# Optimization experiments

Measured on AMD Instinct MI355X. Metric: run time of the kernel, lower is better.

## Reference

```python
import jax, jax.numpy as jnp
import numpy as np

N, E = 50000, 800000
DIM_IN, DIM_H, DIM_OUT, HEADS = 128, 32, 16, 4
HID = DIM_H * HEADS  # 128
FINAL = DIM_OUT * HEADS  # 64
NEG_SLOPE = 0.2


def _glorot(key, shape):
    fan_in, fan_out = shape[0], shape[-1] if len(shape) > 1 else shape[0]
    lim = jnp.sqrt(6.0 / (fan_in + fan_out)).astype(jnp.float32)
    return jax.random.uniform(key, shape, jnp.float32, -lim, lim)


def setup_inputs() -> dict:
    key = jax.random.key(0)
    ks = jax.random.split(key, 16)
    x = jax.random.normal(ks[0], (N, DIM_IN), jnp.float32)
    edge_index = jax.random.randint(ks[1], (2, E), 0, N, dtype=jnp.int64)
    inp = {"x": x, "edge_index": edge_index}
    # layer 1: DIM_IN -> HEADS*DIM_H
    inp["Wl1"] = _glorot(ks[2], (DIM_IN, HEADS * DIM_H))
    inp["Wr1"] = _glorot(ks[3], (DIM_IN, HEADS * DIM_H))
    inp["att1"] = _glorot(ks[4], (HEADS, DIM_H))
    inp["b1"] = jnp.zeros((HEADS * DIM_H,), jnp.float32)
    # layer 2: HID -> HEADS*DIM_H
    inp["Wl2"] = _glorot(ks[5], (HID, HEADS * DIM_H))
    inp["Wr2"] = _glorot(ks[6], (HID, HEADS * DIM_H))
    inp["att2"] = _glorot(ks[7], (HEADS, DIM_H))
    inp["b2"] = jnp.zeros((HEADS * DIM_H,), jnp.float32)
    # layer 3: HID -> HEADS*DIM_OUT
    inp["Wl3"] = _glorot(ks[8], (HID, HEADS * DIM_OUT))
    inp["Wr3"] = _glorot(ks[9], (HID, HEADS * DIM_OUT))
    inp["att3"] = _glorot(ks[10], (HEADS, DIM_OUT))
    inp["b3"] = jnp.zeros((HEADS * DIM_OUT,), jnp.float32)
    return inp


def gatv2_conv(x, src, dst, Wl, Wr, att, b, heads, ch):
    n = x.shape[0]
    xl = (x @ Wl).reshape(n, heads, ch)  # source-side transform
    xr = (x @ Wr).reshape(n, heads, ch)  # target-side transform
    m = xl[src] + xr[dst]                 # [E, H, C]
    e = jnp.einsum('ehc,hc->eh', jax.nn.leaky_relu(m, NEG_SLOPE), att)
    # segment softmax over incoming edges of each dst node
    emax = jax.ops.segment_max(e, dst, num_segments=n)
    ex = jnp.exp(e - emax[dst])
    denom = jax.ops.segment_sum(ex, dst, num_segments=n)
    alpha = ex / denom[dst]               # [E, H]
    out = jax.ops.segment_sum(alpha[:, :, None] * xl[src], dst, num_segments=n)
    return out.reshape(n, heads * ch) + b


def reference(x, edge_index, Wl1, Wr1, att1, b1, Wl2, Wr2, att2, b2, Wl3, Wr3, att3, b3):
    n = x.shape[0]
    loops = jnp.arange(n, dtype=edge_index.dtype)
    src = jnp.concatenate([edge_index[0], loops])  # PyG add_self_loops=True
    dst = jnp.concatenate([edge_index[1], loops])
    # dropout is identity in eval mode
    h = jax.nn.elu(gatv2_conv(x, src, dst, Wl1, Wr1, att1, b1, HEADS, DIM_H))
    h = jax.nn.elu(gatv2_conv(h, src, dst, Wl2, Wr2, att2, b2, HEADS, DIM_H))
    h = gatv2_conv(h, src, dst, Wl3, Wr3, att3, b3, HEADS, DIM_OUT)
    return jax.nn.log_softmax(h, axis=1)
```

## Files before the change

### kernel.cpp

```cpp
#include <hip/hip_runtime.h>
#include <math.h>

constexpr int DIN  = 128;
constexpr int FSH  = 10;
constexpr int NFBM = 64;
constexpr int LCAP = 160;
constexpr int RND  = 4096;
constexpr int FCAP = 18432;

typedef __attribute__((ext_vector_type(8))) short short8;
typedef __attribute__((ext_vector_type(4))) float f32x4;

__device__ __forceinline__ unsigned short f2bf(float f) {
  unsigned u = __float_as_uint(f);
  u = (u + 0x7FFF + ((u >> 16) & 1)) >> 16;
  return (unsigned short)u;
}
__device__ __forceinline__ float bflo(unsigned u) { return __uint_as_float(u << 16); }
__device__ __forceinline__ float bfhi(unsigned u) { return __uint_as_float(u & 0xFFFF0000u); }

__device__ __forceinline__ void unpack8(uint4 u, float* x) {
  x[0] = bflo(u.x); x[1] = bfhi(u.x); x[2] = bflo(u.y); x[3] = bfhi(u.y);
  x[4] = bflo(u.z); x[5] = bfhi(u.z); x[6] = bflo(u.w); x[7] = bfhi(u.w);
}
__device__ __forceinline__ void unpack4(uint2 u, float* x) {
  x[0] = bflo(u.x); x[1] = bfhi(u.x); x[2] = bflo(u.y); x[3] = bfhi(u.y);
}

typedef const __attribute__((address_space(1))) unsigned int guint_t;
typedef __attribute__((address_space(3))) unsigned int luint_t;
__device__ __forceinline__ void async16(const void* g, void* l) {
  __builtin_amdgcn_global_load_lds((guint_t*)g, (luint_t*)l, 16, 0, 0);
}


__global__ __launch_bounds__(256) void bucket_append_kernel(const int* __restrict__ ei,
    int* __restrict__ gcnt, unsigned* __restrict__ gpairs, int E, int nfb) {
  __shared__ unsigned buf[NFBM * LCAP];
  __shared__ int cnt[NFBM];
  __shared__ int gbase[NFBM];
  const int tid = threadIdx.x;
  if (tid < NFBM) cnt[tid] = 0;
  __syncthreads();

  const int k0 = blockIdx.x * RND;
  for (int i = tid; i < RND; i += 256) {
    int k = k0 + i;
    if (k >= E) break;
    int src = ei[k], dst = ei[E + k];
    int fb = dst >> FSH;
    int pos = atomicAdd(&cnt[fb], 1);
    if (pos < LCAP)
      buf[fb * LCAP + pos] = (unsigned)src | ((unsigned)(dst & ((1 << FSH) - 1)) << 16);
  }
  __syncthreads();

  if (tid < nfb) gbase[tid] = atomicAdd(&gcnt[tid], min(cnt[tid], LCAP));
  __syncthreads();

  const int wid = tid >> 6, lane = tid & 63;
  for (int fb = wid; fb < nfb; fb += 4) {
    int c  = min(cnt[fb], LCAP);
    int gb = gbase[fb];
    if (gb >= FCAP) continue;
    c = min(c, FCAP - gb);
    unsigned* dstp = gpairs + (size_t)fb * FCAP + gb;
    const unsigned* srcp = &buf[fb * LCAP];
    for (int i = lane; i < c; i += 64) dstp[i] = srcp[i];
  }
}

__global__ __launch_bounds__(256) void bucket_build_kernel(const unsigned* __restrict__ gpairs,
    const int* __restrict__ gcnt, int* __restrict__ row_ptr,
    int* __restrict__ edge_src, int n, int nfb) {
  const int b   = blockIdx.x;
  const int tid = threadIdx.x;
  const int lane = tid & 63, wid = tid >> 6;
  __shared__ int hist[1024];
  __shared__ int wsum[4];
  __shared__ int base_s;

  const int d0 = b << FSH;
  const int nvalid = min(1 << FSH, n - d0);

  if (wid == 0) {
    int term = 0;
    if (lane < b)
      term = min(gcnt[lane], FCAP) + min(1 << FSH, n - (lane << FSH));
#pragma unroll
    for (int o = 32; o >= 1; o >>= 1) term += __shfl_xor(term, o, 64);
    if (lane == 0) base_s = term;
  }
  for (int i = tid; i < 1024; i += 256) hist[i] = (i < nvalid) ? 1 : 0;
  __syncthreads();

  const int cnt = min(gcnt[b], FCAP);
  const unsigned* bp = gpairs + (size_t)b * FCAP;
  for (int i = tid; i < cnt; i += 256)
    atomicAdd(&hist[bp[i] >> 16], 1);
  __syncthreads();

  const int i4 = tid * 4;
  int h0 = hist[i4], h1 = hist[i4 + 1], h2 = hist[i4 + 2], h3 = hist[i4 + 3];
  int s = h0 + h1 + h2 + h3;
  int incl = s;
#pragma unroll
  for (int o = 1; o < 64; o <<= 1) {
    int t = __shfl_up(incl, o, 64);
    if (lane >= o) incl += t;
  }
  if (lane == 63) wsum[wid] = incl;
  __syncthreads();
  int wo = 0;
  for (int wq = 0; wq < wid; ++wq) wo += wsum[wq];
  const int base = base_s;
  int ex[4];
  ex[0] = wo + incl - s;
  ex[1] = ex[0] + h0;
  ex[2] = ex[1] + h1;
  ex[3] = ex[2] + h2;
#pragma unroll
  for (int j = 0; j < 4; ++j) {
    int d = i4 + j;
    if (d < nvalid) {
      row_ptr[d0 + d] = base + ex[j];
      edge_src[base + ex[j]] = d0 + d;
      hist[d] = ex[j] + 1;
    } else if (d0 + d == n) {
      row_ptr[n] = base + ex[j];
    }
  }
  if (b == nfb - 1 && d0 + 1024 <= n && tid == 0) row_ptr[n] = base + cnt + nvalid;
  __syncthreads();

  for (int i = tid; i < cnt; i += 256) {
    unsigned p = bp[i];
    int pos = atomicAdd(&hist[p >> 16], 1);
    edge_src[base + pos] = (int)(p & 0xFFFFu);
  }
}

__global__ __launch_bounds__(256) void cvt_w_kernel(
    const float* __restrict__ Wl1, const float* __restrict__ Wr1,
    const float* __restrict__ Wl2, const float* __restrict__ Wr2,
    const float* __restrict__ Wl3, const float* __restrict__ Wr3,
    unsigned short* __restrict__ Wt) {
  int e = blockIdx.x * 256 + threadIdx.x;
  if (e >= 81920) return;
  const float* src; int N; int off;
  if (e < 65536) {
    int m = e >> 14; off = e & 16383; N = 128;
    src = (m == 0) ? Wl1 : (m == 1) ? Wr1 : (m == 2) ? Wl2 : Wr2;
  } else {
    int e2 = e - 65536; int m = e2 >> 13; off = e2 & 8191; N = 64;
    src = m ? Wr3 : Wl3;
  }
  int nn = off >> 7, k = off & 127;
  Wt[e] = f2bf(src[(size_t)k * N + nn]);
}


template<int NC, bool CVT>
__global__ __launch_bounds__(256) void gemm2_mfma(const void* __restrict__ Ap,
    const unsigned short* __restrict__ Wlt, const unsigned short* __restrict__ Wrt,
    unsigned short* __restrict__ outl, unsigned short* __restrict__ outr, int M) {
  constexpr int WNB = NC / 16;
  __shared__ char lds[16384 + NC * 256];
  char* As = lds;
  char* Ws = lds + 16384;
  const int tid  = threadIdx.x;
  const int w    = tid >> 6, lane = tid & 63;
  const int q    = lane >> 4, r15 = lane & 15;
  const int row0 = blockIdx.x * 64;

  if constexpr (CVT) {
    const float* Af = (const float*)Ap;
    for (int idx = tid * 4; idx < 64 * 128; idx += 1024) {
      int rl = idx >> 7, k = idx & 127;
      int rg = row0 + rl; if (rg >= M) rg = M - 1;
      float4 v = *(const float4*)&Af[(size_t)rg * 128 + k];
      uint2 pk;
      pk.x = (unsigned)f2bf(v.x) | ((unsigned)f2bf(v.y) << 16);
      pk.y = (unsigned)f2bf(v.z) | ((unsigned)f2bf(v.w) << 16);
      char* addr = As + (rl >> 4) * 4096 + (k >> 5) * 1024 +
                   ((((k >> 3) & 3) * 16) + (rl & 15)) * 16 + (k & 7) * 2;
      *(uint2*)addr = pk;
    }
  } else {
    const unsigned short* A = (const unsigned short*)Ap;
    int r = row0 + w * 16 + r15; if (r >= M) r = M - 1;
    const char* g = (const char*)A + (size_t)r * 256 + q * 16;
    char* l = As + w * 4096;
#pragma unroll
    for (int kk = 0; kk < 4; ++kk) async16(g + kk * 64, l + kk * 1024);
  }
  for (int nt = w; nt < WNB; nt += 4) {
    const char* g = (const char*)Wlt + ((size_t)(nt * 16 + r15)) * 256 + q * 16;
    char* l = Ws + nt * 4096;
#pragma unroll
    for (int kk = 0; kk < 4; ++kk) async16(g + kk * 64, l + kk * 1024);
  }
  __syncthreads();

  const char* aw = As + w * 4096;
  f32x4 acc[WNB] = {};
#pragma unroll
  for (int kk = 0; kk < 4; ++kk) {
    short8 af = *(const short8*)(aw + kk * 1024 + (size_t)lane * 16);
#pragma unroll
    for (int nt = 0; nt < WNB; ++nt) {
      short8 bf = *(const short8*)(Ws + (nt * 4 + kk) * 1024 + (size_t)lane * 16);
      acc[nt] = __builtin_amdgcn_mfma_f32_16x16x32_bf16(af, bf, acc[nt], 0, 0, 0);
    }
  }
  {
    int rowb = row0 + w * 16 + q * 4;
#pragma unroll
    for (int nt = 0; nt < WNB; ++nt)
#pragma unroll
      for (int r = 0; r < 4; ++r) {
        int rr = rowb + r;
        if (rr < M) outl[(size_t)rr * NC + nt * 16 + r15] = f2bf(acc[nt][r]);
      }
  }
  __syncthreads();
  for (int nt = w; nt < WNB; nt += 4) {
    const char* g = (const char*)Wrt + ((size_t)(nt * 16 + r15)) * 256 + q * 16;
    char* l = Ws + nt * 4096;
#pragma unroll
    for (int kk = 0; kk < 4; ++kk) async16(g + kk * 64, l + kk * 1024);
  }
  __syncthreads();

  f32x4 acc2[WNB] = {};
#pragma unroll
  for (int kk = 0; kk < 4; ++kk) {
    short8 af = *(const short8*)(aw + kk * 1024 + (size_t)lane * 16);
#pragma unroll
    for (int nt = 0; nt < WNB; ++nt) {
      short8 bf = *(const short8*)(Ws + (nt * 4 + kk) * 1024 + (size_t)lane * 16);
      acc2[nt] = __builtin_amdgcn_mfma_f32_16x16x32_bf16(af, bf, acc2[nt], 0, 0, 0);
    }
  }
  {
    int rowb = row0 + w * 16 + q * 4;
#pragma unroll
    for (int nt = 0; nt < WNB; ++nt)
#pragma unroll
      for (int r = 0; r < 4; ++r) {
        int rr = rowb + r;
        if (rr < M) outr[(size_t)rr * NC + nt * 16 + r15] = f2bf(acc2[nt][r]);
      }
  }
}


__global__ __launch_bounds__(256) void aggregate128_kernel(
    const unsigned short* __restrict__ xl, const unsigned short* __restrict__ xr,
    const float* __restrict__ att, const float* __restrict__ bias,
    const int* __restrict__ row_ptr, const int* __restrict__ edge_src,
    unsigned short* __restrict__ out, int n) {
  const int tid  = threadIdx.x;
  const int r    = tid & 15;
  const int node = blockIdx.x * 16 + (tid >> 4);
  if (node >= n) return;
  const int c0 = r * 8;

  float xrv[8];
  unpack8(*(const uint4*)&xr[(size_t)node * 128 + c0], xrv);
  float a6[8], a4[8];
  {
    float4 aa = *(const float4*)&att[c0];
    float4 ab = *(const float4*)&att[c0 + 4];
    float at[8] = {aa.x, aa.y, aa.z, aa.w, ab.x, ab.y, ab.z, ab.w};
#pragma unroll
    for (int j = 0; j < 8; ++j) { a6[j] = 0.6f * at[j]; a4[j] = 0.4f * at[j]; }
  }

  float l = 0.f, o[8] = {};
  int idx = row_ptr[node];
  const int end = row_ptr[node + 1];

  for (; idx + 4 <= end; idx += 4) {
    int s0 = edge_src[idx],     s1 = edge_src[idx + 1];
    int s2 = edge_src[idx + 2], s3 = edge_src[idx + 3];
    uint4 u0 = *(const uint4*)&xl[(size_t)s0 * 128 + c0];
    uint4 u1 = *(const uint4*)&xl[(size_t)s1 * 128 + c0];
    uint4 u2 = *(const uint4*)&xl[(size_t)s2 * 128 + c0];
    uint4 u3 = *(const uint4*)&xl[(size_t)s3 * 128 + c0];
    float x0[8], x1[8], x2[8], x3[8];
    unpack8(u0, x0); unpack8(u1, x1); unpack8(u2, x2); unpack8(u3, x3);
    float p0 = 0.f, p1 = 0.f, p2 = 0.f, p3 = 0.f;
#pragma unroll
    for (int j = 0; j < 8; ++j) {
      float t0 = x0[j] + xrv[j], t1 = x1[j] + xrv[j];
      float t2 = x2[j] + xrv[j], t3 = x3[j] + xrv[j];
      p0 = fmaf(t0, a6[j], p0); p0 = fmaf(fabsf(t0), a4[j], p0);
      p1 = fmaf(t1, a6[j], p1); p1 = fmaf(fabsf(t1), a4[j], p1);
      p2 = fmaf(t2, a6[j], p2); p2 = fmaf(fabsf(t2), a4[j], p2);
      p3 = fmaf(t3, a6[j], p3); p3 = fmaf(fabsf(t3), a4[j], p3);
    }
    p0 += __shfl_xor(p0, 1, 64); p0 += __shfl_xor(p0, 2, 64);
    p1 += __shfl_xor(p1, 1, 64); p1 += __shfl_xor(p1, 2, 64);
    p2 += __shfl_xor(p2, 1, 64); p2 += __shfl_xor(p2, 2, 64);
    p3 += __shfl_xor(p3, 1, 64); p3 += __shfl_xor(p3, 2, 64);
    float e0 = __expf(fminf(p0, 80.f)), e1 = __expf(fminf(p1, 80.f));
    float e2 = __expf(fminf(p2, 80.f)), e3 = __expf(fminf(p3, 80.f));
    l += (e0 + e1) + (e2 + e3);
#pragma unroll
    for (int j = 0; j < 8; ++j)
      o[j] = fmaf(e0, x0[j], fmaf(e1, x1[j], fmaf(e2, x2[j], fmaf(e3, x3[j], o[j]))));
  }
  for (; idx < end; ++idx) {
    int s0 = edge_src[idx];
    uint4 u0 = *(const uint4*)&xl[(size_t)s0 * 128 + c0];
    float x0[8];
    unpack8(u0, x0);
    float p0 = 0.f;
#pragma unroll
    for (int j = 0; j < 8; ++j) {
      float t = x0[j] + xrv[j];
      p0 = fmaf(t, a6[j], p0); p0 = fmaf(fabsf(t), a4[j], p0);
    }
    p0 += __shfl_xor(p0, 1, 64); p0 += __shfl_xor(p0, 2, 64);
    float e0 = __expf(fminf(p0, 80.f));
    l += e0;
#pragma unroll
    for (int j = 0; j < 8; ++j) o[j] = fmaf(e0, x0[j], o[j]);
  }

  float4 b0 = *(const float4*)&bias[c0];
  float4 b1 = *(const float4*)&bias[c0 + 4];
  float bb[8] = {b0.x, b0.y, b0.z, b0.w, b1.x, b1.y, b1.z, b1.w};
  unsigned short res[8];
#pragma unroll
  for (int j = 0; j < 8; ++j) {
    float v = o[j] / l + bb[j];
    v = v > 0.f ? v : __expf(v) - 1.f;
    res[j] = f2bf(v);
  }
  uint4 ov;
  ov.x = (unsigned)res[0] | ((unsigned)res[1] << 16);
  ov.y = (unsigned)res[2] | ((unsigned)res[3] << 16);
  ov.z = (unsigned)res[4] | ((unsigned)res[5] << 16);
  ov.w = (unsigned)res[6] | ((unsigned)res[7] << 16);
  *(uint4*)&out[(size_t)node * 128 + c0] = ov;
}


__global__ __launch_bounds__(256) void aggregate64_kernel(
    const unsigned short* __restrict__ xl, const unsigned short* __restrict__ xr,
    const float* __restrict__ att, const float* __restrict__ bias,
    const int* __restrict__ row_ptr, const int* __restrict__ edge_src,
    float* __restrict__ out, int n) {
  const int tid  = threadIdx.x;
  const int r    = tid & 15;
  const int node = blockIdx.x * 16 + (tid >> 4);
  if (node >= n) return;
  const int c0 = r * 4;

  float xrv[4];
  unpack4(*(const uint2*)&xr[(size_t)node * 64 + c0], xrv);
  float a6[4], a4[4];
  {
    float4 aa = *(const float4*)&att[c0];
    float at[4] = {aa.x, aa.y, aa.z, aa.w};
#pragma unroll
    for (int j = 0; j < 4; ++j) { a6[j] = 0.6f * at[j]; a4[j] = 0.4f * at[j]; }
  }

  float l = 0.f, o[4] = {};
  int idx = row_ptr[node];
  const int end = row_ptr[node + 1];

  for (; idx + 4 <= end; idx += 4) {
    int s0 = edge_src[idx],     s1 = edge_src[idx + 1];
    int s2 = edge_src[idx + 2], s3 = edge_src[idx + 3];
    uint2 u0 = *(const uint2*)&xl[(size_t)s0 * 64 + c0];
    uint2 u1 = *(const uint2*)&xl[(size_t)s1 * 64 + c0];
    uint2 u2 = *(const uint2*)&xl[(size_t)s2 * 64 + c0];
    uint2 u3 = *(const uint2*)&xl[(size_t)s3 * 64 + c0];
    float x0[4], x1[4], x2[4], x3[4];
    unpack4(u0, x0); unpack4(u1, x1); unpack4(u2, x2); unpack4(u3, x3);
    float p0 = 0.f, p1 = 0.f, p2 = 0.f, p3 = 0.f;
#pragma unroll
    for (int j = 0; j < 4; ++j) {
      float t0 = x0[j] + xrv[j], t1 = x1[j] + xrv[j];
      float t2 = x2[j] + xrv[j], t3 = x3[j] + xrv[j];
      p0 = fmaf(t0, a6[j], p0); p0 = fmaf(fabsf(t0), a4[j], p0);
      p1 = fmaf(t1, a6[j], p1); p1 = fmaf(fabsf(t1), a4[j], p1);
      p2 = fmaf(t2, a6[j], p2); p2 = fmaf(fabsf(t2), a4[j], p2);
      p3 = fmaf(t3, a6[j], p3); p3 = fmaf(fabsf(t3), a4[j], p3);
    }
    p0 += __shfl_xor(p0, 1, 64); p0 += __shfl_xor(p0, 2, 64);
    p1 += __shfl_xor(p1, 1, 64); p1 += __shfl_xor(p1, 2, 64);
    p2 += __shfl_xor(p2, 1, 64); p2 += __shfl_xor(p2, 2, 64);
    p3 += __shfl_xor(p3, 1, 64); p3 += __shfl_xor(p3, 2, 64);
    float e0 = __expf(fminf(p0, 80.f)), e1 = __expf(fminf(p1, 80.f));
    float e2 = __expf(fminf(p2, 80.f)), e3 = __expf(fminf(p3, 80.f));
    l += (e0 + e1) + (e2 + e3);
#pragma unroll
    for (int j = 0; j < 4; ++j)
      o[j] = fmaf(e0, x0[j], fmaf(e1, x1[j], fmaf(e2, x2[j], fmaf(e3, x3[j], o[j]))));
  }
  for (; idx < end; ++idx) {
    int s0 = edge_src[idx];
    uint2 u0 = *(const uint2*)&xl[(size_t)s0 * 64 + c0];
    float x0[4];
    unpack4(u0, x0);
    float p0 = 0.f;
#pragma unroll
    for (int j = 0; j < 4; ++j) {
      float t = x0[j] + xrv[j];
      p0 = fmaf(t, a6[j], p0); p0 = fmaf(fabsf(t), a4[j], p0);
    }
    p0 += __shfl_xor(p0, 1, 64); p0 += __shfl_xor(p0, 2, 64);
    float e0 = __expf(fminf(p0, 80.f));
    l += e0;
#pragma unroll
    for (int j = 0; j < 4; ++j) o[j] = fmaf(e0, x0[j], o[j]);
  }

  float4 bv = *(const float4*)&bias[c0];
  float bb[4] = {bv.x, bv.y, bv.z, bv.w};
  float rr[4];
#pragma unroll
  for (int j = 0; j < 4; ++j) rr[j] = o[j] / l + bb[j];

  float mx = fmaxf(fmaxf(rr[0], rr[1]), fmaxf(rr[2], rr[3]));
#pragma unroll
  for (int off = 1; off < 16; off <<= 1) mx = fmaxf(mx, __shfl_xor(mx, off, 64));
  float se = __expf(rr[0] - mx) + __expf(rr[1] - mx) +
             __expf(rr[2] - mx) + __expf(rr[3] - mx);
#pragma unroll
  for (int off = 1; off < 16; off <<= 1) se += __shfl_xor(se, off, 64);
  float ls = mx + __logf(se);
  *(float4*)&out[(size_t)node * 64 + c0] =
      make_float4(rr[0] - ls, rr[1] - ls, rr[2] - ls, rr[3] - ls);
}


extern "C" void kernel_launch(void* const* d_in, const int* in_sizes, int n_in,
                              void* d_out, int out_size, void* d_ws, size_t ws_size,
                              hipStream_t stream) {
  const float* x    = (const float*)d_in[0];
  const int*   ei   = (const int*)d_in[1];
  const float* Wl1  = (const float*)d_in[2];
  const float* Wr1  = (const float*)d_in[3];
  const float* att1 = (const float*)d_in[4];
  const float* b1   = (const float*)d_in[5];
  const float* Wl2  = (const float*)d_in[6];
  const float* Wr2  = (const float*)d_in[7];
  const float* att2 = (const float*)d_in[8];
  const float* b2   = (const float*)d_in[9];
  const float* Wl3  = (const float*)d_in[10];
  const float* Wr3  = (const float*)d_in[11];
  const float* att3 = (const float*)d_in[12];
  const float* b3   = (const float*)d_in[13];
  const int n = in_sizes[0] / DIN;
  const int E = in_sizes[1] / 2;
  float* out = (float*)d_out;

  const int nfb = (n + (1 << FSH) - 1) >> FSH;

  unsigned short* xl = (unsigned short*)d_ws;
  unsigned short* xr = xl + (size_t)n * 128;
  unsigned short* h  = xr + (size_t)n * 128;
  unsigned short* Wt = h + (size_t)n * 128;
  unsigned short* Wl1t = Wt, *Wr1t = Wt + 16384;
  unsigned short* Wl2t = Wt + 32768, *Wr2t = Wt + 49152;
  unsigned short* Wl3t = Wt + 65536, *Wr3t = Wt + 73728;
  int* row_ptr  = (int*)(Wt + 81920);
  int* gcnt     = row_ptr + (n + 16);
  int* edge_src = gcnt + NFBM;
  unsigned* gpairs = (unsigned*)(edge_src + (((size_t)E + n + 15) & ~(size_t)15));

  cvt_w_kernel<<<320, 256, 0, stream>>>(Wl1, Wr1, Wl2, Wr2, Wl3, Wr3, Wt);

  hipMemsetAsync(gcnt, 0, NFBM * sizeof(int), stream);
  bucket_append_kernel<<<(E + RND - 1) / RND, 256, 0, stream>>>(ei, gcnt, gpairs, E, nfb);
  bucket_build_kernel<<<nfb, 256, 0, stream>>>(gpairs, gcnt, row_ptr, edge_src, n, nfb);

  const int gb = (n + 63) / 64;
  const int ab = (n + 15) / 16;

  gemm2_mfma<128, true><<<gb, 256, 0, stream>>>(x, Wl1t, Wr1t, xl, xr, n);
  aggregate128_kernel<<<ab, 256, 0, stream>>>(xl, xr, att1, b1, row_ptr, edge_src, h, n);
  gemm2_mfma<128, false><<<gb, 256, 0, stream>>>(h, Wl2t, Wr2t, xl, xr, n);
  aggregate128_kernel<<<ab, 256, 0, stream>>>(xl, xr, att2, b2, row_ptr, edge_src, h, n);
  gemm2_mfma<64, false><<<gb, 256, 0, stream>>>(h, Wl3t, Wr3t, xl, xr, n);
  aggregate64_kernel<<<ab, 256, 0, stream>>>(xl, xr, att3, b3, row_ptr, edge_src, out, n);
}
```

Measured before the change: 298.3 us.

## Pack edge sources to 16-bit, vectorize aggregation math, fold memset into weight conversion

```diff
diff --git a/kernel.cpp b/kernel.cpp
--- a/kernel.cpp
+++ b/kernel.cpp
@@ -10,6 +10,7 @@
 
 typedef __attribute__((ext_vector_type(8))) short short8;
 typedef __attribute__((ext_vector_type(4))) float f32x4;
+typedef __attribute__((ext_vector_type(2))) float f32x2;
 
 __device__ __forceinline__ unsigned short f2bf(float f) {
   unsigned u = __float_as_uint(f);
@@ -18,19 +19,48 @@
 }
 __device__ __forceinline__ float bflo(unsigned u) { return __uint_as_float(u << 16); }
 __device__ __forceinline__ float bfhi(unsigned u) { return __uint_as_float(u & 0xFFFF0000u); }
-
-__device__ __forceinline__ void unpack8(uint4 u, float* x) {
-  x[0] = bflo(u.x); x[1] = bfhi(u.x); x[2] = bflo(u.y); x[3] = bfhi(u.y);
-  x[4] = bflo(u.z); x[5] = bfhi(u.z); x[6] = bflo(u.w); x[7] = bfhi(u.w);
-}
-__device__ __forceinline__ void unpack4(uint2 u, float* x) {
-  x[0] = bflo(u.x); x[1] = bfhi(u.x); x[2] = bflo(u.y); x[3] = bfhi(u.y);
+__device__ __forceinline__ f32x2 bfpair(unsigned u) {
+  f32x2 r; r.x = bflo(u); r.y = bfhi(u); return r;
+}
+__device__ __forceinline__ f32x2 fabs2(f32x2 v) {
+  f32x2 r; r.x = fabsf(v.x); r.y = fabsf(v.y); return r;
 }
 
 typedef const __attribute__((address_space(1))) unsigned int guint_t;
 typedef __attribute__((address_space(3))) unsigned int luint_t;
 __device__ __forceinline__ void async16(const void* g, void* l) {
   __builtin_amdgcn_global_load_lds((guint_t*)g, (luint_t*)l, 16, 0, 0);
+}
+
+__device__ __forceinline__ float score8(uint4 u, const f32x2* xrp,
+                                        const f32x2* a6, const f32x2* a4, f32x2* xp) {
+  xp[0] = bfpair(u.x); xp[1] = bfpair(u.y);
+  xp[2] = bfpair(u.z); xp[3] = bfpair(u.w);
+  f32x2 acc = {0.f, 0.f};
+#pragma unroll
+  for (int j = 0; j < 4; ++j) {
+    f32x2 t = xp[j] + xrp[j];
+    acc += t * a6[j] + fabs2(t) * a4[j];
+  }
+  float p = acc.x + acc.y;
+  p += __shfl_xor(p, 1, 64);
+  p += __shfl_xor(p, 2, 64);
+  return p;
+}
+
+__device__ __forceinline__ float score4(uint2 u, const f32x2* xrp,
+                                        const f32x2* a6, const f32x2* a4, f32x2* xp) {
+  xp[0] = bfpair(u.x); xp[1] = bfpair(u.y);
+  f32x2 acc = {0.f, 0.f};
+#pragma unroll
+  for (int j = 0; j < 2; ++j) {
+    f32x2 t = xp[j] + xrp[j];
+    acc += t * a6[j] + fabs2(t) * a4[j];
+  }
+  float p = acc.x + acc.y;
+  p += __shfl_xor(p, 1, 64);
+  p += __shfl_xor(p, 2, 64);
+  return p;
 }
 
 
@@ -72,7 +102,7 @@
 
 __global__ __launch_bounds__(256) void bucket_build_kernel(const unsigned* __restrict__ gpairs,
     const int* __restrict__ gcnt, int* __restrict__ row_ptr,
-    int* __restrict__ edge_src, int n, int nfb) {
+    unsigned short* __restrict__ edge_src, int n, int nfb) {
   const int b   = blockIdx.x;
   const int tid = threadIdx.x;
   const int lane = tid & 63, wid = tid >> 6;
@@ -124,7 +154,7 @@
     int d = i4 + j;
     if (d < nvalid) {
       row_ptr[d0 + d] = base + ex[j];
-      edge_src[base + ex[j]] = d0 + d;
+      edge_src[base + ex[j]] = (unsigned short)(d0 + d);
       hist[d] = ex[j] + 1;
     } else if (d0 + d == n) {
       row_ptr[n] = base + ex[j];
@@ -136,7 +166,7 @@
   for (int i = tid; i < cnt; i += 256) {
     unsigned p = bp[i];
     int pos = atomicAdd(&hist[p >> 16], 1);
-    edge_src[base + pos] = (int)(p & 0xFFFFu);
+    edge_src[base + pos] = (unsigned short)(p & 0xFFFFu);
   }
 }
 
@@ -144,7 +174,8 @@
     const float* __restrict__ Wl1, const float* __restrict__ Wr1,
     const float* __restrict__ Wl2, const float* __restrict__ Wr2,
     const float* __restrict__ Wl3, const float* __restrict__ Wr3,
-    unsigned short* __restrict__ Wt) {
+    unsigned short* __restrict__ Wt, int* __restrict__ gcnt) {
+  if (blockIdx.x == 0 && threadIdx.x < NFBM) gcnt[threadIdx.x] = 0;
   int e = blockIdx.x * 256 + threadIdx.x;
   if (e >= 81920) return;
   const float* src; int N; int off;
@@ -258,7 +289,7 @@
 __global__ __launch_bounds__(256) void aggregate128_kernel(
     const unsigned short* __restrict__ xl, const unsigned short* __restrict__ xr,
     const float* __restrict__ att, const float* __restrict__ bias,
-    const int* __restrict__ row_ptr, const int* __restrict__ edge_src,
+    const int* __restrict__ row_ptr, const unsigned short* __restrict__ edge_src,
     unsigned short* __restrict__ out, int n) {
   const int tid  = threadIdx.x;
   const int r    = tid & 15;
@@ -266,18 +297,26 @@
   if (node >= n) return;
   const int c0 = r * 8;
 
-  float xrv[8];
-  unpack8(*(const uint4*)&xr[(size_t)node * 128 + c0], xrv);
-  float a6[8], a4[8];
+  f32x2 xrp[4];
+  {
+    uint4 u = *(const uint4*)&xr[(size_t)node * 128 + c0];
+    xrp[0] = bfpair(u.x); xrp[1] = bfpair(u.y);
+    xrp[2] = bfpair(u.z); xrp[3] = bfpair(u.w);
+  }
+  f32x2 a6[4], a4[4];
   {
     float4 aa = *(const float4*)&att[c0];
     float4 ab = *(const float4*)&att[c0 + 4];
     float at[8] = {aa.x, aa.y, aa.z, aa.w, ab.x, ab.y, ab.z, ab.w};
 #pragma unroll
-    for (int j = 0; j < 8; ++j) { a6[j] = 0.6f * at[j]; a4[j] = 0.4f * at[j]; }
-  }
-
-  float l = 0.f, o[8] = {};
+    for (int j = 0; j < 4; ++j) {
+      a6[j].x = 0.6f * at[2 * j];     a6[j].y = 0.6f * at[2 * j + 1];
+      a4[j].x = 0.4f * at[2 * j];     a4[j].y = 0.4f * at[2 * j + 1];
+    }
+  }
+
+  float l = 0.f;
+  f32x2 o[4] = {};
   int idx = row_ptr[node];
   const int end = row_ptr[node + 1];
 
@@ -288,56 +327,43 @@
     uint4 u1 = *(const uint4*)&xl[(size_t)s1 * 128 + c0];
     uint4 u2 = *(const uint4*)&xl[(size_t)s2 * 128 + c0];
     uint4 u3 = *(const uint4*)&xl[(size_t)s3 * 128 + c0];
-    float x0[8], x1[8], x2[8], x3[8];
-    unpack8(u0, x0); unpack8(u1, x1); unpack8(u2, x2); unpack8(u3, x3);
-    float p0 = 0.f, p1 = 0.f, p2 = 0.f, p3 = 0.f;
-#pragma unroll
-    for (int j = 0; j < 8; ++j) {
-      float t0 = x0[j] + xrv[j], t1 = x1[j] + xrv[j];
-      float t2 = x2[j] + xrv[j], t3 = x3[j] + xrv[j];
-      p0 = fmaf(t0, a6[j], p0); p0 = fmaf(fabsf(t0), a4[j], p0);
-      p1 = fmaf(t1, a6[j], p1); p1 = fmaf(fabsf(t1), a4[j], p1);
-      p2 = fmaf(t2, a6[j], p2); p2 = fmaf(fabsf(t2), a4[j], p2);
-      p3 = fmaf(t3, a6[j], p3); p3 = fmaf(fabsf(t3), a4[j], p3);
-    }
-    p0 += __shfl_xor(p0, 1, 64); p0 += __shfl_xor(p0, 2, 64);
-    p1 += __shfl_xor(p1, 1, 64); p1 += __shfl_xor(p1, 2, 64);
-    p2 += __shfl_xor(p2, 1, 64); p2 += __shfl_xor(p2, 2, 64);
-    p3 += __shfl_xor(p3, 1, 64); p3 += __shfl_xor(p3, 2, 64);
+    f32x2 x0[4], x1[4], x2[4], x3[4];
+    float p0 = score8(u0, xrp, a6, a4, x0);
+    float p1 = score8(u1, xrp, a6, a4, x1);
+    float p2 = score8(u2, xrp, a6, a4, x2);
+    float p3 = score8(u3, xrp, a6, a4, x3);
     float e0 = __expf(fminf(p0, 80.f)), e1 = __expf(fminf(p1, 80.f));
     float e2 = __expf(fminf(p2, 80.f)), e3 = __expf(fminf(p3, 80.f));
     l += (e0 + e1) + (e2 + e3);
-#pragma unroll
-    for (int j = 0; j < 8; ++j)
-      o[j] = fmaf(e0, x0[j], fmaf(e1, x1[j], fmaf(e2, x2[j], fmaf(e3, x3[j], o[j]))));
+    f32x2 ev0 = {e0, e0}, ev1 = {e1, e1}, ev2 = {e2, e2}, ev3 = {e3, e3};
+#pragma unroll
+    for (int j = 0; j < 4; ++j)
+      o[j] += ev0 * x0[j] + ev1 * x1[j] + ev2 * x2[j] + ev3 * x3[j];
   }
   for (; idx < end; ++idx) {
     int s0 = edge_src[idx];
     uint4 u0 = *(const uint4*)&xl[(size_t)s0 * 128 + c0];
-    float x0[8];
-    unpack8(u0, x0);
-    float p0 = 0.f;
-#pragma unroll
-    for (int j = 0; j < 8; ++j) {
-      float t = x0[j] + xrv[j];
-      p0 = fmaf(t, a6[j], p0); p0 = fmaf(fabsf(t), a4[j], p0);
-    }
-    p0 += __shfl_xor(p0, 1, 64); p0 += __shfl_xor(p0, 2, 64);
+    f32x2 x0[4];
+    float p0 = score8(u0, xrp, a6, a4, x0);
     float e0 = __expf(fminf(p0, 80.f));
     l += e0;
-#pragma unroll
-    for (int j = 0; j < 8; ++j) o[j] = fmaf(e0, x0[j], o[j]);
+    f32x2 ev0 = {e0, e0};
+#pragma unroll
+    for (int j = 0; j < 4; ++j) o[j] += ev0 * x0[j];
   }
 
   float4 b0 = *(const float4*)&bias[c0];
   float4 b1 = *(const float4*)&bias[c0 + 4];
   float bb[8] = {b0.x, b0.y, b0.z, b0.w, b1.x, b1.y, b1.z, b1.w};
+  float rl = 1.f / l;
   unsigned short res[8];
 #pragma unroll
-  for (int j = 0; j < 8; ++j) {
-    float v = o[j] / l + bb[j];
-    v = v > 0.f ? v : __expf(v) - 1.f;
-    res[j] = f2bf(v);
+  for (int j = 0; j < 4; ++j) {
+    float v0 = o[j].x * rl + bb[2 * j];
+    float v1 = o[j].y * rl + bb[2 * j + 1];
+    v0 = v0 > 0.f ? v0 : __expf(v0) - 1.f;
+    v1 = v1 > 0.f ? v1 : __expf(v1) - 1.f;
+    res[2 * j] = f2bf(v0); res[2 * j + 1] = f2bf(v1);
   }
   uint4 ov;
   ov.x = (unsigned)res[0] | ((unsigned)res[1] << 16);
@@ -351,7 +377,7 @@
 __global__ __launch_bounds__(256) void aggregate64_kernel(
     const unsigned short* __restrict__ xl, const unsigned short* __restrict__ xr,
     const float* __restrict__ att, const float* __restrict__ bias,
-    const int* __restrict__ row_ptr, const int* __restrict__ edge_src,
+    const int* __restrict__ row_ptr, const unsigned short* __restrict__ edge_src,
     float* __restrict__ out, int n) {
   const int tid  = threadIdx.x;
   const int r    = tid & 15;
@@ -359,17 +385,22 @@
   if (node >= n) return;
   const int c0 = r * 4;
 
-  float xrv[4];
-  unpack4(*(const uint2*)&xr[(size_t)node * 64 + c0], xrv);
-  float a6[4], a4[4];
+  f32x2 xrp[2];
+  {
+    uint2 u = *(const uint2*)&xr[(size_t)node * 64 + c0];
+    xrp[0] = bfpair(u.x); xrp[1] = bfpair(u.y);
+  }
+  f32x2 a6[2], a4[2];
   {
     float4 aa = *(const float4*)&att[c0];
-    float at[4] = {aa.x, aa.y, aa.z, aa.w};
-#pragma unroll
-    for (int j = 0; j < 4; ++j) { a6[j] = 0.6f * at[j]; a4[j] = 0.4f * at[j]; }
-  }
-
-  float l = 0.f, o[4] = {};
+    a6[0].x = 0.6f * aa.x; a6[0].y = 0.6f * aa.y;
+    a6[1].x = 0.6f * aa.z; a6[1].y = 0.6f * aa.w;
+    a4[0].x = 0.4f * aa.x; a4[0].y = 0.4f * aa.y;
+    a4[1].x = 0.4f * aa.z; a4[1].y = 0.4f * aa.w;
+  }
+
+  float l = 0.f;
+  f32x2 o[2] = {};
   int idx = row_ptr[node];
   const int end = row_ptr[node + 1];
 
@@ -380,52 +411,38 @@
     uint2 u1 = *(const uint2*)&xl[(size_t)s1 * 64 + c0];
     uint2 u2 = *(const uint2*)&xl[(size_t)s2 * 64 + c0];
     uint2 u3 = *(const uint2*)&xl[(size_t)s3 * 64 + c0];
-    float x0[4], x1[4], x2[4], x3[4];
-    unpack4(u0, x0); unpack4(u1, x1); unpack4(u2, x2); unpack4(u3, x3);
-    float p0 = 0.f, p1 = 0.f, p2 = 0.f, p3 = 0.f;
-#pragma unroll
-    for (int j = 0; j < 4; ++j) {
-      float t0 = x0[j] + xrv[j], t1 = x1[j] + xrv[j];
-      float t2 = x2[j] + xrv[j], t3 = x3[j] + xrv[j];
-      p0 = fmaf(t0, a6[j], p0); p0 = fmaf(fabsf(t0), a4[j], p0);
-      p1 = fmaf(t1, a6[j], p1); p1 = fmaf(fabsf(t1), a4[j], p1);
-      p2 = fmaf(t2, a6[j], p2); p2 = fmaf(fabsf(t2), a4[j], p2);
-      p3 = fmaf(t3, a6[j], p3); p3 = fmaf(fabsf(t3), a4[j], p3);
-    }
-    p0 += __shfl_xor(p0, 1, 64); p0 += __shfl_xor(p0, 2, 64);
-    p1 += __shfl_xor(p1, 1, 64); p1 += __shfl_xor(p1, 2, 64);
-    p2 += __shfl_xor(p2, 1, 64); p2 += __shfl_xor(p2, 2, 64);
-    p3 += __shfl_xor(p3, 1, 64); p3 += __shfl_xor(p3, 2, 64);
+    f32x2 x0[2], x1[2], x2[2], x3[2];
+    float p0 = score4(u0, xrp, a6, a4, x0);
+    float p1 = score4(u1, xrp, a6, a4, x1);
+    float p2 = score4(u2, xrp, a6, a4, x2);
+    float p3 = score4(u3, xrp, a6, a4, x3);
     float e0 = __expf(fminf(p0, 80.f)), e1 = __expf(fminf(p1, 80.f));
     float e2 = __expf(fminf(p2, 80.f)), e3 = __expf(fminf(p3, 80.f));
     l += (e0 + e1) + (e2 + e3);
-#pragma unroll
-    for (int j = 0; j < 4; ++j)
-      o[j] = fmaf(e0, x0[j], fmaf(e1, x1[j], fmaf(e2, x2[j], fmaf(e3, x3[j], o[j]))));
+    f32x2 ev0 = {e0, e0}, ev1 = {e1, e1}, ev2 = {e2, e2}, ev3 = {e3, e3};
+#pragma unroll
+    for (int j = 0; j < 2; ++j)
+      o[j] += ev0 * x0[j] + ev1 * x1[j] + ev2 * x2[j] + ev3 * x3[j];
   }
   for (; idx < end; ++idx) {
     int s0 = edge_src[idx];
     uint2 u0 = *(const uint2*)&xl[(size_t)s0 * 64 + c0];
-    float x0[4];
-    unpack4(u0, x0);
-    float p0 = 0.f;
-#pragma unroll
-    for (int j = 0; j < 4; ++j) {
-      float t = x0[j] + xrv[j];
-      p0 = fmaf(t, a6[j], p0); p0 = fmaf(fabsf(t), a4[j], p0);
-    }
-    p0 += __shfl_xor(p0, 1, 64); p0 += __shfl_xor(p0, 2, 64);
+    f32x2 x0[2];
+    float p0 = score4(u0, xrp, a6, a4, x0);
     float e0 = __expf(fminf(p0, 80.f));
     l += e0;
-#pragma unroll
-    for (int j = 0; j < 4; ++j) o[j] = fmaf(e0, x0[j], o[j]);
+    f32x2 ev0 = {e0, e0};
+#pragma unroll
+    for (int j = 0; j < 2; ++j) o[j] += ev0 * x0[j];
   }
 
   float4 bv = *(const float4*)&bias[c0];
-  float bb[4] = {bv.x, bv.y, bv.z, bv.w};
+  float rl = 1.f / l;
   float rr[4];
-#pragma unroll
-  for (int j = 0; j < 4; ++j) rr[j] = o[j] / l + bb[j];
+  rr[0] = o[0].x * rl + bv.x;
+  rr[1] = o[0].y * rl + bv.y;
+  rr[2] = o[1].x * rl + bv.z;
+  rr[3] = o[1].y * rl + bv.w;
 
   float mx = fmaxf(fmaxf(rr[0], rr[1]), fmaxf(rr[2], rr[3]));
 #pragma unroll
@@ -472,12 +489,12 @@
   unsigned short* Wl3t = Wt + 65536, *Wr3t = Wt + 73728;
   int* row_ptr  = (int*)(Wt + 81920);
   int* gcnt     = row_ptr + (n + 16);
-  int* edge_src = gcnt + NFBM;
-  unsigned* gpairs = (unsigned*)(edge_src + (((size_t)E + n + 15) & ~(size_t)15));
-
-  cvt_w_kernel<<<320, 256, 0, stream>>>(Wl1, Wr1, Wl2, Wr2, Wl3, Wr3, Wt);
-
-  hipMemsetAsync(gcnt, 0, NFBM * sizeof(int), stream);
+  unsigned short* edge_src = (unsigned short*)(gcnt + NFBM);
+  unsigned* gpairs = (unsigned*)((char*)edge_src +
+      ((((size_t)(E + n) * 2) + 15) & ~(size_t)15));
+
+  cvt_w_kernel<<<320, 256, 0, stream>>>(Wl1, Wr1, Wl2, Wr2, Wl3, Wr3, Wt, gcnt);
+
   bucket_append_kernel<<<(E + RND - 1) / RND, 256, 0, stream>>>(ei, gcnt, gpairs, E, nfb);
   bucket_build_kernel<<<nfb, 256, 0, stream>>>(gpairs, gcnt, row_ptr, edge_src, n, nfb);
 
```

Measured after the change: 311.5 us. +4.4%, slower.
